# Performance work log

Measured on AMD Instinct MI355X. Metric: run time of the kernel, lower is better.

## Reference

```python
import jax, jax.numpy as jnp
import numpy as np

N_EMBD = 384
HEAD_SIZE = 64
B, T = 4, 4096
SCALE = HEAD_SIZE ** -0.5

def setup_inputs() -> dict:
    key = jax.random.key(0)
    kx, kq, kk, kv = jax.random.split(key, 4)
    x = jax.random.normal(kx, (B, T, N_EMBD), dtype=jnp.float32)
    # nn.Linear(n_embd, head_size, bias=False): store as [in, out] for x @ W
    s = 1.0 / np.sqrt(N_EMBD)
    Wq = jax.random.normal(kq, (N_EMBD, HEAD_SIZE), dtype=jnp.float32) * s
    Wk = jax.random.normal(kk, (N_EMBD, HEAD_SIZE), dtype=jnp.float32) * s
    Wv = jax.random.normal(kv, (N_EMBD, HEAD_SIZE), dtype=jnp.float32) * s
    return {"x": x, "Wq": Wq, "Wk": Wk, "Wv": Wv}

def reference(x, Wq, Wk, Wv):
    # q,k,v: [B,T,H]
    q = jnp.einsum("btc,ch->bth", x, Wq)
    k = jnp.einsum("btc,ch->bth", x, Wk)
    v = jnp.einsum("btc,ch->bth", x, Wv)
    # scores: [B,T,T], causal masked, scaled by head_size**-0.5
    wei = jnp.einsum("bqh,bkh->bqk", q, k) * SCALE
    tq = jnp.arange(q.shape[1])
    causal = tq[:, None] >= tq[None, :]  # [T,T] lower-triangular
    wei = jnp.where(causal[None, :, :], wei, -jnp.inf)
    wei = jax.nn.softmax(wei, axis=-1)
    # dropout omitted (eval / deterministic reference)
    out = jnp.einsum("bqk,bkh->bqh", wei, v)
    return out
```

## Files before the change

### kernel.cpp

```cpp
#include <hip/hip_runtime.h>

#define BATCH 4
#define SEQ   4096
#define NEMBD 384
#define HDIM  64
#define KBLK  64
#define QSCALE 0.18033688011112042f
#define NEG_BIG (-1.0e30f)
#define DEFER_THR 8.0f
#define EXP2F(x) __builtin_amdgcn_exp2f(x)

__global__ __launch_bounds__(512) void qkv_proj_kernel(
    const float* __restrict__ x,
    const float* __restrict__ Wq,
    const float* __restrict__ Wk,
    const float* __restrict__ Wv,
    float* __restrict__ q,
    float* __restrict__ k,
    float* __restrict__ v)
{
    __shared__ float xs[32][NEMBD];
    const int tid  = threadIdx.x;
    const long row0 = (long)blockIdx.x * 32;

    {
        const float4* xg = (const float4*)(x + row0*NEMBD);
        float4* xl = (float4*)&xs[0][0];
#pragma unroll
        for (int i = 0; i < 6; ++i)
            xl[tid + i*512] = xg[tid + i*512];
    }
    __syncthreads();

    const int c  = tid & 63;
    const int rg = tid >> 6;
    float aq[4], ak[4], av[4];
#pragma unroll
    for (int r = 0; r < 4; ++r) { aq[r]=0.f; ak[r]=0.f; av[r]=0.f; }

#pragma unroll 2
    for (int k4 = 0; k4 < NEMBD/4; ++k4) {
        const int kk = k4*4;
        float4 xr[4];
#pragma unroll
        for (int r = 0; r < 4; ++r)
            xr[r] = *(const float4*)&xs[rg*4 + r][kk];
#pragma unroll
        for (int jj = 0; jj < 4; ++jj) {
            const float wq = Wq[(kk+jj)*HDIM + c];
            const float wk = Wk[(kk+jj)*HDIM + c];
            const float wv = Wv[(kk+jj)*HDIM + c];
#pragma unroll
            for (int r = 0; r < 4; ++r) {
                const float xc = (jj==0)?xr[r].x:(jj==1)?xr[r].y:(jj==2)?xr[r].z:xr[r].w;
                aq[r] = fmaf(xc, wq, aq[r]);
                ak[r] = fmaf(xc, wk, ak[r]);
                av[r] = fmaf(xc, wv, av[r]);
            }
        }
    }
#pragma unroll
    for (int r = 0; r < 4; ++r) {
        const long o = (row0 + rg*4 + r)*HDIM + c;
        q[o] = aq[r];
        k[o] = ak[r];
        v[o] = av[r];
    }
}

__device__ __forceinline__ float red8(float x) {
    int t = __builtin_amdgcn_update_dpp(0, __float_as_int(x), 0xB1, 0xF, 0xF, true);
    x += __int_as_float(t);
    t = __builtin_amdgcn_update_dpp(0, __float_as_int(x), 0x4E, 0xF, 0xF, true);
    x += __int_as_float(t);
    t = __builtin_amdgcn_update_dpp(0, __float_as_int(x), 0x141, 0xF, 0xF, true);
    x += __int_as_float(t);
    return x;
}


#define KEYSTEP(MASKED)                                                        \
  {                                                                            \
    const float4 ka = *(const float4*)&Ks[kk][j8];                             \
    const float4 kb = *(const float4*)&Ks[kk][j8 + 4];                         \
    float s[4];                                                                \
    _Pragma("unroll")                                                          \
    for (int r = 0; r < 4; ++r) {                                              \
      float acc =       qa[r].x * ka.x;                                        \
      acc = fmaf(qa[r].y, ka.y, acc);                                          \
      acc = fmaf(qa[r].z, ka.z, acc);                                          \
      acc = fmaf(qa[r].w, ka.w, acc);                                          \
      acc = fmaf(qb[r].x, kb.x, acc);                                          \
      acc = fmaf(qb[r].y, kb.y, acc);                                          \
      acc = fmaf(qb[r].z, kb.z, acc);                                          \
      acc = fmaf(qb[r].w, kb.w, acc);                                          \
      s[r] = red8(acc);                                                        \
    }                                                                          \
    const float c = fmaxf(fmaxf(s[0]-m[0], s[1]-m[1]),                         \
                          fmaxf(s[2]-m[2], s[3]-m[3]));                        \
    if (__any(c > DEFER_THR)) {                                      \
      _Pragma("unroll")                                                        \
      for (int r = 0; r < 4; ++r) {                                            \
        const float nm = fmaxf(m[r], s[r]);                                    \
        const float sc = EXP2F(m[r] - nm);                                     \
        m[r] = nm; l[r] *= sc;                                                 \
        oa[r].x *= sc; oa[r].y *= sc; oa[r].z *= sc; oa[r].w *= sc;            \
        ob[r].x *= sc; ob[r].y *= sc; ob[r].z *= sc; ob[r].w *= sc;            \
      }                                                                        \
    }                                                                          \
    const float4 va = *(const float4*)&Vs[kk][j8];                             \
    const float4 vb = *(const float4*)&Vs[kk][j8 + 4];                         \
    _Pragma("unroll")                                                          \
    for (int r = 0; r < 4; ++r) {                                              \
      float p = EXP2F(s[r] - m[r]);                                            \
      if (MASKED) p = (base + kk <= r0 + r) ? p : 0.f;                         \
      l[r] += p;                                                               \
      oa[r].x = fmaf(p, va.x, oa[r].x); oa[r].y = fmaf(p, va.y, oa[r].y);      \
      oa[r].z = fmaf(p, va.z, oa[r].z); oa[r].w = fmaf(p, va.w, oa[r].w);      \
      ob[r].x = fmaf(p, vb.x, ob[r].x); ob[r].y = fmaf(p, vb.y, ob[r].y);      \
      ob[r].z = fmaf(p, vb.z, ob[r].z); ob[r].w = fmaf(p, vb.w, ob[r].w);      \
    }                                                                          \
  }

__global__ __launch_bounds__(256, 4) void attn_kernel(
    const float* __restrict__ Q,
    const float* __restrict__ K,
    const float* __restrict__ V,
    float* __restrict__ opart,
    float* __restrict__ mlpart,
    const int S)
{
    __shared__ float Ks[KBLK][HDIM];
    __shared__ float Vs[KBLK][HDIM];

    const int gid  = blockIdx.x;
    const int part = gid % S;
    const int rest = gid / S;
    const int b    = rest & 3;
    const int qt   = 31 - (rest >> 2);
    const int q0   = qt * 128;
    const int tid  = threadIdx.x;
    const int w    = tid >> 6;
    const int lane = tid & 63;
    const int g    = lane >> 3;
    const int j8   = (lane & 7) * 8;
    const int Rw   = q0 + w*32;
    const int r0   = Rw + g*4;
    const int wmax = Rw + 31;

    float4 qa[4], qb[4];
    {
        const float* qp = Q + ((long)b*SEQ + r0)*HDIM + j8;
#pragma unroll
        for (int r = 0; r < 4; ++r) {
            float4 t = *(const float4*)(qp + r*HDIM);
            qa[r].x = t.x*QSCALE; qa[r].y = t.y*QSCALE;
            qa[r].z = t.z*QSCALE; qa[r].w = t.w*QSCALE;
            t = *(const float4*)(qp + r*HDIM + 4);
            qb[r].x = t.x*QSCALE; qb[r].y = t.y*QSCALE;
            qb[r].z = t.z*QSCALE; qb[r].w = t.w*QSCALE;
        }
    }
    float4 oa[4], ob[4];
    float m[4], l[4];
#pragma unroll
    for (int r = 0; r < 4; ++r) {
        oa[r].x=0.f; oa[r].y=0.f; oa[r].z=0.f; oa[r].w=0.f;
        ob[r].x=0.f; ob[r].y=0.f; ob[r].z=0.f; ob[r].w=0.f;
        m[r] = NEG_BIG; l[r] = 0.f;
    }

    const float* Kb = K + (long)b*SEQ*HDIM;
    const float* Vb = V + (long)b*SEQ*HDIM;
    const int ntiles = (q0 + 128) / KBLK;

    for (int kt = part; kt < ntiles; kt += S) {
        __syncthreads();
        {
            const float4* Kg = (const float4*)(Kb + (long)kt*KBLK*HDIM);
            const float4* Vg = (const float4*)(Vb + (long)kt*KBLK*HDIM);
            float4* Ksw = (float4*)&Ks[0][0];
            float4* Vsw = (float4*)&Vs[0][0];
#pragma unroll
            for (int i = 0; i < 4; ++i) {
                Ksw[tid + i*256] = Kg[tid + i*256];
                Vsw[tid + i*256] = Vg[tid + i*256];
            }
        }
        __syncthreads();

        const int base = kt * KBLK;
        if (base > wmax) continue;

        if (base + KBLK <= Rw) {
            for (int kk = 0; kk < KBLK; ++kk) KEYSTEP(false)
        } else {
            const int kkend = Rw + 32 - base;
            for (int kk = 0; kk < kkend; ++kk) KEYSTEP(true)
        }
    }

    const long PERM = (long)BATCH * SEQ;
    const long obase = ((long)part*PERM + (long)b*SEQ + r0)*HDIM + j8;
#pragma unroll
    for (int r = 0; r < 4; ++r) {
        *(float4*)(opart + obase + r*HDIM)     = oa[r];
        *(float4*)(opart + obase + r*HDIM + 4) = ob[r];
    }
    if (j8 == 0) {
#pragma unroll
        for (int r = 0; r < 4; ++r) {
            float2 ml; ml.x = m[r]; ml.y = l[r];
            *(float2*)&mlpart[((long)part*PERM + (long)b*SEQ + r0 + r)*2] = ml;
        }
    }
}

__global__ __launch_bounds__(256) void combine_kernel(
    const float* __restrict__ opart,
    const float* __restrict__ mlpart,
    float* __restrict__ out,
    const int S)
{
    const int tid  = threadIdx.x;
    const int d    = tid & 63;
    const int rsub = tid >> 6;
    const long row = (long)blockIdx.x * 4 + rsub;
    const long PERO = (long)BATCH * SEQ * HDIM;
    const long PERM = (long)BATCH * SEQ;

    float M = NEG_BIG;
    for (int p = 0; p < S; ++p)
        M = fmaxf(M, mlpart[((long)p*PERM + row)*2]);

    float L = 0.f, acc = 0.f;
    for (int p = 0; p < S; ++p) {
        const float2 ml = *(const float2*)&mlpart[((long)p*PERM + row)*2];
        const float e = EXP2F(ml.x - M);
        L   = fmaf(ml.y, e, L);
        acc = fmaf(opart[(long)p*PERO + row*HDIM + d], e, acc);
    }
    out[row*HDIM + d] = acc / L;
}

extern "C" void kernel_launch(void* const* d_in, const int* in_sizes, int n_in,
                              void* d_out, int out_size, void* d_ws, size_t ws_size,
                              hipStream_t stream) {
    const float* x  = (const float*)d_in[0];
    const float* Wq = (const float*)d_in[1];
    const float* Wk = (const float*)d_in[2];
    const float* Wv = (const float*)d_in[3];
    float* out = (float*)d_out;

    const size_t PER  = (size_t)BATCH * SEQ * HDIM;
    const size_t PERM = (size_t)BATCH * SEQ;

    int S = 8;
    while (S > 1 && (3*PER + (size_t)S*PER + (size_t)S*PERM*2)*4 > ws_size) S >>= 1;

    float* qws    = (float*)d_ws;
    float* kws    = qws + PER;
    float* vws    = kws + PER;
    float* opart  = vws + PER;
    float* mlpart = opart + (size_t)S*PER;

    qkv_proj_kernel<<<BATCH*SEQ/32, 512, 0, stream>>>(x, Wq, Wk, Wv, qws, kws, vws);
    attn_kernel<<<S*BATCH*(SEQ/128), 256, 0, stream>>>(qws, kws, vws, opart, mlpart, S);
    combine_kernel<<<BATCH*SEQ/4, 256, 0, stream>>>(opart, mlpart, out, S);
}
```

Measured before the change: 310.5 us.

## Pack attention math into float2 packed FMAs, prefetch weights, raise split count

The attention inner loop is rewritten on two-wide float vectors so the compiler can emit packed FP32 FMA instructions (v_pk_fma_f32) for the QK dot products, the rescale and the PV accumulation. This targets the VALU instruction count of the FP32 scalar path. Separately, the QKV projection now runs 16 rows per 256-thread block and prefetches the next group of weights into registers. The split-K factor S doubles to 16, which adds partial-output traffic and combine work in exchange for more parallel attention blocks.

After: 367.1 us. 18.2% more time.

```diff
diff --git a/kernel.cpp b/kernel.cpp
--- a/kernel.cpp
+++ b/kernel.cpp
@@ -10,7 +10,15 @@
 #define DEFER_THR 8.0f
 #define EXP2F(x) __builtin_amdgcn_exp2f(x)
 
-__global__ __launch_bounds__(512) void qkv_proj_kernel(
+typedef float f32x2 __attribute__((ext_vector_type(2)));
+
+__device__ __forceinline__ f32x2 splat2(float s) { f32x2 r; r.x = s; r.y = s; return r; }
+__device__ __forceinline__ f32x2 mk2(float a, float b) { f32x2 r; r.x = a; r.y = b; return r; }
+__device__ __forceinline__ f32x2 fma2(f32x2 a, f32x2 b, f32x2 c) {
+    return __builtin_elementwise_fma(a, b, c);
+}
+
+__global__ __launch_bounds__(256) void qkv_proj_kernel(
     const float* __restrict__ x,
     const float* __restrict__ Wq,
     const float* __restrict__ Wk,
@@ -19,16 +27,16 @@
     float* __restrict__ k,
     float* __restrict__ v)
 {
-    __shared__ float xs[32][NEMBD];
+    __shared__ float xs[16][NEMBD];
     const int tid  = threadIdx.x;
-    const long row0 = (long)blockIdx.x * 32;
+    const long row0 = (long)blockIdx.x * 16;
 
     {
         const float4* xg = (const float4*)(x + row0*NEMBD);
         float4* xl = (float4*)&xs[0][0];
 #pragma unroll
         for (int i = 0; i < 6; ++i)
-            xl[tid + i*512] = xg[tid + i*512];
+            xl[tid + i*256] = xg[tid + i*256];
     }
     __syncthreads();
 
@@ -38,26 +46,44 @@
 #pragma unroll
     for (int r = 0; r < 4; ++r) { aq[r]=0.f; ak[r]=0.f; av[r]=0.f; }
 
+    const float* pq = Wq + c;
+    const float* pk = Wk + c;
+    const float* pv = Wv + c;
+
+    float wq[4], wk[4], wv[4];
+#pragma unroll
+    for (int jj = 0; jj < 4; ++jj) {
+        wq[jj] = pq[jj*HDIM]; wk[jj] = pk[jj*HDIM]; wv[jj] = pv[jj*HDIM];
+    }
+
 #pragma unroll 2
     for (int k4 = 0; k4 < NEMBD/4; ++k4) {
         const int kk = k4*4;
+        float nwq[4], nwk[4], nwv[4];
+        if (k4 + 1 < NEMBD/4) {
+#pragma unroll
+            for (int jj = 0; jj < 4; ++jj) {
+                nwq[jj] = pq[(kk+4+jj)*HDIM];
+                nwk[jj] = pk[(kk+4+jj)*HDIM];
+                nwv[jj] = pv[(kk+4+jj)*HDIM];
+            }
+        }
         float4 xr[4];
 #pragma unroll
         for (int r = 0; r < 4; ++r)
             xr[r] = *(const float4*)&xs[rg*4 + r][kk];
 #pragma unroll
         for (int jj = 0; jj < 4; ++jj) {
-            const float wq = Wq[(kk+jj)*HDIM + c];
-            const float wk = Wk[(kk+jj)*HDIM + c];
-            const float wv = Wv[(kk+jj)*HDIM + c];
 #pragma unroll
             for (int r = 0; r < 4; ++r) {
                 const float xc = (jj==0)?xr[r].x:(jj==1)?xr[r].y:(jj==2)?xr[r].z:xr[r].w;
-                aq[r] = fmaf(xc, wq, aq[r]);
-                ak[r] = fmaf(xc, wk, ak[r]);
-                av[r] = fmaf(xc, wv, av[r]);
+                aq[r] = fmaf(xc, wq[jj], aq[r]);
+                ak[r] = fmaf(xc, wk[jj], ak[r]);
+                av[r] = fmaf(xc, wv[jj], av[r]);
             }
         }
+#pragma unroll
+        for (int jj = 0; jj < 4; ++jj) { wq[jj]=nwq[jj]; wk[jj]=nwk[jj]; wv[jj]=nwv[jj]; }
     }
 #pragma unroll
     for (int r = 0; r < 4; ++r) {
@@ -79,47 +105,66 @@
 }
 
 
+#define DOT_PAIR(P, KA, KB, OUT)                                               \
+    { f32x2 t = q2##P[0] * KA.x;                                               \
+      t = fma2(q2##P[1], splat2(KA.y), t);                                     \
+      t = fma2(q2##P[2], splat2(KA.z), t);                                     \
+      t = fma2(q2##P[3], splat2(KA.w), t);                                     \
+      t = fma2(q2##P[4], splat2(KB.x), t);                                     \
+      t = fma2(q2##P[5], splat2(KB.y), t);                                     \
+      t = fma2(q2##P[6], splat2(KB.z), t);                                     \
+      t = fma2(q2##P[7], splat2(KB.w), t);                                     \
+      OUT = t; }
+
 #define KEYSTEP(MASKED)                                                        \
   {                                                                            \
     const float4 ka = *(const float4*)&Ks[kk][j8];                             \
     const float4 kb = *(const float4*)&Ks[kk][j8 + 4];                         \
-    float s[4];                                                                \
-    _Pragma("unroll")                                                          \
-    for (int r = 0; r < 4; ++r) {                                              \
-      float acc =       qa[r].x * ka.x;                                        \
-      acc = fmaf(qa[r].y, ka.y, acc);                                          \
-      acc = fmaf(qa[r].z, ka.z, acc);                                          \
-      acc = fmaf(qa[r].w, ka.w, acc);                                          \
-      acc = fmaf(qb[r].x, kb.x, acc);                                          \
-      acc = fmaf(qb[r].y, kb.y, acc);                                          \
-      acc = fmaf(qb[r].z, kb.z, acc);                                          \
-      acc = fmaf(qb[r].w, kb.w, acc);                                          \
-      s[r] = red8(acc);                                                        \
+    f32x2 a0, a1;                                                              \
+    DOT_PAIR(0, ka, kb, a0)                                                    \
+    DOT_PAIR(1, ka, kb, a1)                                                    \
+    f32x2 s20 = mk2(red8(a0.x), red8(a0.y));                                   \
+    f32x2 s21 = mk2(red8(a1.x), red8(a1.y));                                   \
+    const f32x2 d0 = s20 - m20, d1 = s21 - m21;                                \
+    const float cmax = fmaxf(fmaxf(d0.x, d0.y), fmaxf(d1.x, d1.y));            \
+    if (__any(cmax > DEFER_THR)) {                                   \
+      f32x2 nm0 = __builtin_elementwise_max(m20, s20);                         \
+      f32x2 nm1 = __builtin_elementwise_max(m21, s21);                         \
+      f32x2 sc0 = mk2(EXP2F(m20.x - nm0.x), EXP2F(m20.y - nm0.y));             \
+      f32x2 sc1 = mk2(EXP2F(m21.x - nm1.x), EXP2F(m21.y - nm1.y));             \
+      m20 = nm0; m21 = nm1;                                                    \
+      l20 = l20 * sc0; l21 = l21 * sc1;                                        \
+      _Pragma("unroll")                                                        \
+      for (int d = 0; d < 8; ++d) { o20[d] = o20[d]*sc0; o21[d] = o21[d]*sc1; }\
     }                                                                          \
-    const float c = fmaxf(fmaxf(s[0]-m[0], s[1]-m[1]),                         \
-                          fmaxf(s[2]-m[2], s[3]-m[3]));                        \
-    if (__any(c > DEFER_THR)) {                                      \
-      _Pragma("unroll")                                                        \
-      for (int r = 0; r < 4; ++r) {                                            \
-        const float nm = fmaxf(m[r], s[r]);                                    \
-        const float sc = EXP2F(m[r] - nm);                                     \
-        m[r] = nm; l[r] *= sc;                                                 \
-        oa[r].x *= sc; oa[r].y *= sc; oa[r].z *= sc; oa[r].w *= sc;            \
-        ob[r].x *= sc; ob[r].y *= sc; ob[r].z *= sc; ob[r].w *= sc;            \
-      }                                                                        \
+    f32x2 pp0 = mk2(EXP2F(s20.x - m20.x), EXP2F(s20.y - m20.y));               \
+    f32x2 pp1 = mk2(EXP2F(s21.x - m21.x), EXP2F(s21.y - m21.y));               \
+    if (MASKED) {                                                              \
+      const int doff = base + kk - r0;                    \
+      pp0.x = (doff <= 0) ? pp0.x : 0.f;                                       \
+      pp0.y = (doff <= 1) ? pp0.y : 0.f;                                       \
+      pp1.x = (doff <= 2) ? pp1.x : 0.f;                                       \
+      pp1.y = (doff <= 3) ? pp1.y : 0.f;                                       \
     }                                                                          \
+    l20 += pp0; l21 += pp1;                                                    \
     const float4 va = *(const float4*)&Vs[kk][j8];                             \
     const float4 vb = *(const float4*)&Vs[kk][j8 + 4];                         \
-    _Pragma("unroll")                                                          \
-    for (int r = 0; r < 4; ++r) {                                              \
-      float p = EXP2F(s[r] - m[r]);                                            \
-      if (MASKED) p = (base + kk <= r0 + r) ? p : 0.f;                         \
-      l[r] += p;                                                               \
-      oa[r].x = fmaf(p, va.x, oa[r].x); oa[r].y = fmaf(p, va.y, oa[r].y);      \
-      oa[r].z = fmaf(p, va.z, oa[r].z); oa[r].w = fmaf(p, va.w, oa[r].w);      \
-      ob[r].x = fmaf(p, vb.x, ob[r].x); ob[r].y = fmaf(p, vb.y, ob[r].y);      \
-      ob[r].z = fmaf(p, vb.z, ob[r].z); ob[r].w = fmaf(p, vb.w, ob[r].w);      \
-    }                                                                          \
+    o20[0] = fma2(pp0, splat2(va.x), o20[0]);                                  \
+    o20[1] = fma2(pp0, splat2(va.y), o20[1]);                                  \
+    o20[2] = fma2(pp0, splat2(va.z), o20[2]);                                  \
+    o20[3] = fma2(pp0, splat2(va.w), o20[3]);                                  \
+    o20[4] = fma2(pp0, splat2(vb.x), o20[4]);                                  \
+    o20[5] = fma2(pp0, splat2(vb.y), o20[5]);                                  \
+    o20[6] = fma2(pp0, splat2(vb.z), o20[6]);                                  \
+    o20[7] = fma2(pp0, splat2(vb.w), o20[7]);                                  \
+    o21[0] = fma2(pp1, splat2(va.x), o21[0]);                                  \
+    o21[1] = fma2(pp1, splat2(va.y), o21[1]);                                  \
+    o21[2] = fma2(pp1, splat2(va.z), o21[2]);                                  \
+    o21[3] = fma2(pp1, splat2(va.w), o21[3]);                                  \
+    o21[4] = fma2(pp1, splat2(vb.x), o21[4]);                                  \
+    o21[5] = fma2(pp1, splat2(vb.y), o21[5]);                                  \
+    o21[6] = fma2(pp1, splat2(vb.z), o21[6]);                                  \
+    o21[7] = fma2(pp1, splat2(vb.w), o21[7]);                                  \
   }
 
 __global__ __launch_bounds__(256, 4) void attn_kernel(
@@ -148,27 +193,31 @@
     const int r0   = Rw + g*4;
     const int wmax = Rw + 31;
 
-    float4 qa[4], qb[4];
+    f32x2 q20[8], q21[8];
     {
         const float* qp = Q + ((long)b*SEQ + r0)*HDIM + j8;
-#pragma unroll
-        for (int r = 0; r < 4; ++r) {
-            float4 t = *(const float4*)(qp + r*HDIM);
-            qa[r].x = t.x*QSCALE; qa[r].y = t.y*QSCALE;
-            qa[r].z = t.z*QSCALE; qa[r].w = t.w*QSCALE;
-            t = *(const float4*)(qp + r*HDIM + 4);
-            qb[r].x = t.x*QSCALE; qb[r].y = t.y*QSCALE;
-            qb[r].z = t.z*QSCALE; qb[r].w = t.w*QSCALE;
-        }
-    }
-    float4 oa[4], ob[4];
-    float m[4], l[4];
-#pragma unroll
-    for (int r = 0; r < 4; ++r) {
-        oa[r].x=0.f; oa[r].y=0.f; oa[r].z=0.f; oa[r].w=0.f;
-        ob[r].x=0.f; ob[r].y=0.f; ob[r].z=0.f; ob[r].w=0.f;
-        m[r] = NEG_BIG; l[r] = 0.f;
-    }
+        const float4 A0 = *(const float4*)(qp);
+        const float4 B0 = *(const float4*)(qp + 4);
+        const float4 A1 = *(const float4*)(qp + HDIM);
+        const float4 B1 = *(const float4*)(qp + HDIM + 4);
+        const float4 A2 = *(const float4*)(qp + 2*HDIM);
+        const float4 B2 = *(const float4*)(qp + 2*HDIM + 4);
+        const float4 A3 = *(const float4*)(qp + 3*HDIM);
+        const float4 B3 = *(const float4*)(qp + 3*HDIM + 4);
+        q20[0] = mk2(A0.x, A1.x) * QSCALE; q20[1] = mk2(A0.y, A1.y) * QSCALE;
+        q20[2] = mk2(A0.z, A1.z) * QSCALE; q20[3] = mk2(A0.w, A1.w) * QSCALE;
+        q20[4] = mk2(B0.x, B1.x) * QSCALE; q20[5] = mk2(B0.y, B1.y) * QSCALE;
+        q20[6] = mk2(B0.z, B1.z) * QSCALE; q20[7] = mk2(B0.w, B1.w) * QSCALE;
+        q21[0] = mk2(A2.x, A3.x) * QSCALE; q21[1] = mk2(A2.y, A3.y) * QSCALE;
+        q21[2] = mk2(A2.z, A3.z) * QSCALE; q21[3] = mk2(A2.w, A3.w) * QSCALE;
+        q21[4] = mk2(B2.x, B3.x) * QSCALE; q21[5] = mk2(B2.y, B3.y) * QSCALE;
+        q21[6] = mk2(B2.z, B3.z) * QSCALE; q21[7] = mk2(B2.w, B3.w) * QSCALE;
+    }
+    f32x2 o20[8], o21[8];
+    f32x2 m20 = splat2(NEG_BIG), m21 = splat2(NEG_BIG);
+    f32x2 l20 = splat2(0.f),     l21 = splat2(0.f);
+#pragma unroll
+    for (int d = 0; d < 8; ++d) { o20[d] = splat2(0.f); o21[d] = splat2(0.f); }
 
     const float* Kb = K + (long)b*SEQ*HDIM;
     const float* Vb = V + (long)b*SEQ*HDIM;
@@ -202,17 +251,35 @@
 
     const long PERM = (long)BATCH * SEQ;
     const long obase = ((long)part*PERM + (long)b*SEQ + r0)*HDIM + j8;
-#pragma unroll
-    for (int r = 0; r < 4; ++r) {
-        *(float4*)(opart + obase + r*HDIM)     = oa[r];
-        *(float4*)(opart + obase + r*HDIM + 4) = ob[r];
+    {
+        float4 ra, rb;
+        ra.x = o20[0].x; ra.y = o20[1].x; ra.z = o20[2].x; ra.w = o20[3].x;
+        rb.x = o20[4].x; rb.y = o20[5].x; rb.z = o20[6].x; rb.w = o20[7].x;
+        *(float4*)(opart + obase)              = ra;
+        *(float4*)(opart + obase + 4)          = rb;
+        ra.x = o20[0].y; ra.y = o20[1].y; ra.z = o20[2].y; ra.w = o20[3].y;
+        rb.x = o20[4].y; rb.y = o20[5].y; rb.z = o20[6].y; rb.w = o20[7].y;
+        *(float4*)(opart + obase + HDIM)       = ra;
+        *(float4*)(opart + obase + HDIM + 4)   = rb;
+        ra.x = o21[0].x; ra.y = o21[1].x; ra.z = o21[2].x; ra.w = o21[3].x;
+        rb.x = o21[4].x; rb.y = o21[5].x; rb.z = o21[6].x; rb.w = o21[7].x;
+        *(float4*)(opart + obase + 2*HDIM)     = ra;
+        *(float4*)(opart + obase + 2*HDIM + 4) = rb;
+        ra.x = o21[0].y; ra.y = o21[1].y; ra.z = o21[2].y; ra.w = o21[3].y;
+        rb.x = o21[4].y; rb.y = o21[5].y; rb.z = o21[6].y; rb.w = o21[7].y;
+        *(float4*)(opart + obase + 3*HDIM)     = ra;
+        *(float4*)(opart + obase + 3*HDIM + 4) = rb;
     }
     if (j8 == 0) {
-#pragma unroll
-        for (int r = 0; r < 4; ++r) {
-            float2 ml; ml.x = m[r]; ml.y = l[r];
-            *(float2*)&mlpart[((long)part*PERM + (long)b*SEQ + r0 + r)*2] = ml;
-        }
+        float2 ml;
+        ml.x = m20.x; ml.y = l20.x;
+        *(float2*)&mlpart[((long)part*PERM + (long)b*SEQ + r0 + 0)*2] = ml;
+        ml.x = m20.y; ml.y = l20.y;
+        *(float2*)&mlpart[((long)part*PERM + (long)b*SEQ + r0 + 1)*2] = ml;
+        ml.x = m21.x; ml.y = l21.x;
+        *(float2*)&mlpart[((long)part*PERM + (long)b*SEQ + r0 + 2)*2] = ml;
+        ml.x = m21.y; ml.y = l21.y;
+        *(float2*)&mlpart[((long)part*PERM + (long)b*SEQ + r0 + 3)*2] = ml;
     }
 }
 
@@ -255,7 +322,7 @@
     const size_t PER  = (size_t)BATCH * SEQ * HDIM;
     const size_t PERM = (size_t)BATCH * SEQ;
 
-    int S = 8;
+    int S = 16;
     while (S > 1 && (3*PER + (size_t)S*PER + (size_t)S*PERM*2)*4 > ws_size) S >>= 1;
 
     float* qws    = (float*)d_ws;
@@ -264,7 +331,7 @@
     float* opart  = vws + PER;
     float* mlpart = opart + (size_t)S*PER;
 
-    qkv_proj_kernel<<<BATCH*SEQ/32, 512, 0, stream>>>(x, Wq, Wk, Wv, qws, kws, vws);
+    qkv_proj_kernel<<<BATCH*SEQ/16, 256, 0, stream>>>(x, Wq, Wk, Wv, qws, kws, vws);
     attn_kernel<<<S*BATCH*(SEQ/128), 256, 0, stream>>>(qws, kws, vws, opart, mlpart, S);
     combine_kernel<<<BATCH*SEQ/4, 256, 0, stream>>>(opart, mlpart, out, S);
 }
```
